# Optimization experiments

Measured on AMD Instinct MI355X. Metric: run time of the kernel, lower is better.

## Reference

```python
import jax, jax.numpy as jnp
import numpy as np

D_MODEL = 512
HEADS = 8
FF_HIDDEN = 1024
EPS = 1e-6


def setup_inputs() -> dict:
    key = jax.random.key(0)
    ks = jax.random.split(key, 12)
    s = 1.0 / np.sqrt(D_MODEL)
    inp = {
        'x': jax.random.normal(ks[0], (2, 4096, D_MODEL), dtype=jnp.float32),
        'Wq': jax.random.normal(ks[1], (D_MODEL, D_MODEL), dtype=jnp.float32) * s,
        'bq': jnp.zeros((D_MODEL,), jnp.float32),
        'Wk': jax.random.normal(ks[2], (D_MODEL, D_MODEL), dtype=jnp.float32) * s,
        'bk': jnp.zeros((D_MODEL,), jnp.float32),
        'Wv': jax.random.normal(ks[3], (D_MODEL, D_MODEL), dtype=jnp.float32) * s,
        'bv': jnp.zeros((D_MODEL,), jnp.float32),
        'Wo': jax.random.normal(ks[4], (D_MODEL, D_MODEL), dtype=jnp.float32) * s,
        'bo': jnp.zeros((D_MODEL,), jnp.float32),
        'a1': jnp.ones((D_MODEL,), jnp.float32),
        'b1': jnp.zeros((D_MODEL,), jnp.float32),
        'a2': jnp.ones((D_MODEL,), jnp.float32),
        'b2': jnp.zeros((D_MODEL,), jnp.float32),
        'W1': jax.random.normal(ks[5], (D_MODEL, FF_HIDDEN), dtype=jnp.float32) * s,
        'c1': jnp.zeros((FF_HIDDEN,), jnp.float32),
        'W2': jax.random.normal(ks[6], (FF_HIDDEN, D_MODEL), dtype=jnp.float32) * (1.0 / np.sqrt(FF_HIDDEN)),
        'c2': jnp.zeros((D_MODEL,), jnp.float32),
    }
    return inp


def _layer_norm(x, a, b):
    # Faithful to source: uses unbiased std (torch default) and divides by (std + eps)
    mean = jnp.mean(x, axis=-1, keepdims=True)
    std = jnp.std(x, axis=-1, keepdims=True, ddof=1)
    return a * ((x - mean) / (std + EPS)) + b


def _encoder_block(x, Wq, bq, Wk, bk, Wv, bv, Wo, bo, a1, b1, a2, b2, W1, c1, W2, c2):
    B, S, D = x.shape
    H, dk = HEADS, D // HEADS
    q = (x @ Wq + bq).reshape(B, S, H, dk).transpose(0, 2, 1, 3)  # [B,H,S,dk]
    k = (x @ Wk + bk).reshape(B, S, H, dk).transpose(0, 2, 1, 3)
    v = (x @ Wv + bv).reshape(B, S, H, dk).transpose(0, 2, 1, 3)
    scores = jnp.einsum('bhqd,bhkd->bhqk', q, k) / np.sqrt(dk)
    probs = jax.nn.softmax(scores, axis=-1)
    attn = jnp.einsum('bhqk,bhkd->bhqd', probs, v)
    concat = attn.transpose(0, 2, 1, 3).reshape(B, S, D)
    attn_out = concat @ Wo + bo
    x = _layer_norm(x + attn_out, a1, b1)  # dropout = identity (eval mode)
    ffn = jax.nn.relu(x @ W1 + c1) @ W2 + c2
    return _layer_norm(x + ffn, a2, b2)


def reference(x, Wq, bq, Wk, bk, Wv, bv, Wo, bo, a1, b1, a2, b2, W1, c1, W2, c2):
    return _encoder_block(x, Wq, bq, Wk, bk, Wv, bv, Wo, bo, a1, b1, a2, b2, W1, c1, W2, c2)
```

## Files before the change

kernel.cpp:

```cpp
#include <hip/hip_runtime.h>
#include <stdint.h>

typedef short short8 __attribute__((ext_vector_type(8)));
typedef short short4v __attribute__((ext_vector_type(4)));
typedef float f32x4 __attribute__((ext_vector_type(4)));
typedef float f32x16 __attribute__((ext_vector_type(16)));
typedef unsigned int u32x4 __attribute__((ext_vector_type(4)));

#define LOG2E 1.44269504088896f
#define QSCALE (0.125f * LOG2E)

__device__ __forceinline__ unsigned short f2b(float f) {
  union { float f; unsigned int u; } x; x.f = f;
  unsigned int u = x.u;
  unsigned int r = (u + 0x7fffu + ((u >> 16) & 1u)) >> 16;
  return (unsigned short)r;
}
__device__ __forceinline__ float b2f(unsigned short s) {
  union { unsigned int u; float f; } x; x.u = ((unsigned int)s) << 16;
  return x.f;
}
__device__ __forceinline__ void gl16(const void* g, void* l) {
  __builtin_amdgcn_global_load_lds((const __attribute__((address_space(1))) void*)g,
                                   (__attribute__((address_space(3))) void*)l, 16, 0, 0);
}
__device__ __forceinline__ unsigned int cvtpk(float lo, float hi) {
  unsigned int r;
  asm("v_cvt_pk_bf16_f32 %0, %1, %2" : "=v"(r) : "v"(lo), "v"(hi));
  return r;
}
__device__ __forceinline__ void plswap(unsigned int& a, unsigned int& b) {
  asm volatile("v_permlane32_swap_b32 %0, %1" : "+v"(a), "+v"(b));
}

__global__ __launch_bounds__(256) void castx_k(const float* __restrict__ X,
                                               unsigned short* __restrict__ Xb) {
  int i = blockIdx.x * 256 + threadIdx.x;
  const float* p = X + (size_t)i * 8;
  float4 a = *(const float4*)(p);
  float4 b = *(const float4*)(p + 4);
  short8 o;
  o[0] = (short)f2b(a.x); o[1] = (short)f2b(a.y);
  o[2] = (short)f2b(a.z); o[3] = (short)f2b(a.w);
  o[4] = (short)f2b(b.x); o[5] = (short)f2b(b.y);
  o[6] = (short)f2b(b.z); o[7] = (short)f2b(b.w);
  *(short8*)(Xb + (size_t)i * 8) = o;
}

__global__ __launch_bounds__(256) void catb_k(const float* __restrict__ bq,
                                              const float* __restrict__ bk,
                                              const float* __restrict__ bv,
                                              float* __restrict__ Bqkv) {
  for (int i = threadIdx.x; i < 1536; i += 256) {
    float v = (i < 512) ? bq[i] * QSCALE : (i < 1024 ? bk[i - 512] : bv[i - 1024]);
    Bqkv[i] = v;
  }
}

__global__ __launch_bounds__(256) void wtrans_k(const float* __restrict__ W,
                                                unsigned short* __restrict__ WT,
                                                int K, int N, float scale) {
  __shared__ float t[64][65];
  int k0 = blockIdx.x * 64, n0 = blockIdx.y * 64;
  for (int i = threadIdx.x; i < 4096; i += 256) {
    int r = i >> 6, c = i & 63;
    t[r][c] = W[(size_t)(k0 + r) * N + n0 + c];
  }
  __syncthreads();
  for (int i = threadIdx.x; i < 4096; i += 256) {
    int r = i >> 6, c = i & 63;
    WT[(size_t)(n0 + r) * K + k0 + c] = f2b(t[c][r] * scale);
  }
}

template <int EPI>
__global__ __launch_bounds__(256) void gemm_bt(
    const unsigned short* __restrict__ A, const unsigned short* __restrict__ BT,
    const float* __restrict__ bias, float* __restrict__ Cf,
    unsigned short* __restrict__ Cb, int M, int N, int K) {
  __shared__ unsigned short As[128 * 32];
  __shared__ unsigned short Bs[128 * 32];
  int t = threadIdx.x, w = t >> 6, l = t & 63;
  int bm = blockIdx.x, bn = blockIdx.y;
  int wm = w >> 1, wn = w & 1;
  int g = l >> 4, ln = l & 15;
  f32x4 acc[4][4] = {};
  const unsigned short* Arow = A + (size_t)bm * 128 * K;
  const unsigned short* Brow = BT + (size_t)bn * 128 * K;
  int nk = K >> 5;
  for (int kt = 0; kt < nk; ++kt) {
    int k0 = kt * 32;
#pragma unroll
    for (int i = 0; i < 2; ++i) {
      int cl = i * 256 + t;
      int r = cl >> 2, c = cl & 3;
      char* ldsA = (char*)As + (size_t)(i * 256 + w * 64) * 16;
      char* ldsB = (char*)Bs + (size_t)(i * 256 + w * 64) * 16;
      gl16(Arow + (size_t)r * K + k0 + c * 8, ldsA);
      gl16(Brow + (size_t)r * K + k0 + c * 8, ldsB);
    }
    __syncthreads();
    short8 af[4], bf[4];
    int ko = g * 8;
#pragma unroll
    for (int i = 0; i < 4; ++i)
      af[i] = *(const short8*)&As[(wm * 64 + i * 16 + ln) * 32 + ko];
#pragma unroll
    for (int j = 0; j < 4; ++j)
      bf[j] = *(const short8*)&Bs[(wn * 64 + j * 16 + ln) * 32 + ko];
    __builtin_amdgcn_s_setprio(1);
#pragma unroll
    for (int i = 0; i < 4; ++i)
#pragma unroll
      for (int j = 0; j < 4; ++j)
        acc[i][j] = __builtin_amdgcn_mfma_f32_16x16x32_bf16(af[i], bf[j], acc[i][j], 0, 0, 0);
    __builtin_amdgcn_s_setprio(0);
    __syncthreads();
  }
#pragma unroll
  for (int i = 0; i < 4; ++i) {
    int row = bm * 128 + wm * 64 + i * 16 + g * 4;
#pragma unroll
    for (int j = 0; j < 4; ++j) {
      int col = bn * 128 + wn * 64 + j * 16 + ln;
      float bv = bias[col];
      float vv[4];
#pragma unroll
      for (int r = 0; r < 4; ++r) {
        float v = acc[i][j][r] + bv;
        if constexpr (EPI == 2) v = v > 0.f ? v : 0.f;
        vv[r] = v;
      }
      if constexpr (EPI == 3) {
        if (col < 1024) {
#pragma unroll
          for (int r = 0; r < 4; ++r)
            Cb[(size_t)(col >> 9) * 4194304 + (size_t)(row + r) * 512 + (col & 511)] = f2b(vv[r]);
        } else {
          short4v pk;
#pragma unroll
          for (int r = 0; r < 4; ++r) pk[r] = (short)f2b(vv[r]);
          *(short4v*)((unsigned short*)Cf +
                      (size_t)((row >> 12) * 512 + (col & 511)) * 4096 + (row & 4095)) = pk;
        }
      } else {
#pragma unroll
        for (int r = 0; r < 4; ++r)
          Cb[(size_t)(row + r) * N + col] = f2b(vv[r]);
      }
    }
  }
}

template <bool WB>
__global__ __launch_bounds__(512) void gemmln_k(
    const unsigned short* __restrict__ A, const unsigned short* __restrict__ BT,
    const float* __restrict__ bias, const float* __restrict__ X,
    const float* __restrict__ gamma, const float* __restrict__ beta,
    float* __restrict__ outf, unsigned short* __restrict__ outb, int K) {
  __shared__ unsigned short As[16 * 32];
  __shared__ unsigned short Bs[512 * 32];
  __shared__ float stats[8][16][2];
  __shared__ float minv[16][2];
  int tid = threadIdx.x, wv = tid >> 6, lane = tid & 63;
  int g = lane >> 4, ln = lane & 15;
  int bm = blockIdx.x;
  f32x4 acc[4] = {};
  const unsigned short* Arow = A + (size_t)bm * 16 * K;
  int nk = K >> 5;
  for (int kt = 0; kt < nk; ++kt) {
    int k0 = kt * 32;
    if (tid < 64) {
      int r = tid >> 2, c = tid & 3;
      gl16(Arow + (size_t)r * K + k0 + c * 8, (char*)As + tid * 16);
    }
#pragma unroll
    for (int i = 0; i < 4; ++i) {
      int u = i * 512 + tid;
      int r = u >> 2, c = u & 3;
      gl16(BT + (size_t)r * K + k0 + c * 8, (char*)Bs + (size_t)u * 16);
    }
    __syncthreads();
    short8 af = *(const short8*)&As[ln * 32 + g * 8];
    __builtin_amdgcn_s_setprio(1);
#pragma unroll
    for (int j = 0; j < 4; ++j) {
      short8 bf = *(const short8*)&Bs[(wv * 64 + j * 16 + ln) * 32 + g * 8];
      acc[j] = __builtin_amdgcn_mfma_f32_16x16x32_bf16(af, bf, acc[j], 0, 0, 0);
    }
    __builtin_amdgcn_s_setprio(0);
    __syncthreads();
  }
  int row0 = bm * 16;
  float v[4][4];
  float ps[4] = {0.f, 0.f, 0.f, 0.f}, pss[4] = {0.f, 0.f, 0.f, 0.f};
#pragma unroll
  for (int j = 0; j < 4; ++j) {
    int col = wv * 64 + j * 16 + ln;
    float bv = bias[col];
#pragma unroll
    for (int r = 0; r < 4; ++r) {
      float t = acc[j][r] + bv + X[(size_t)(row0 + g * 4 + r) * 512 + col];
      v[j][r] = t;
      ps[r] += t; pss[r] += t * t;
    }
  }
#pragma unroll
  for (int off = 1; off < 16; off <<= 1) {
#pragma unroll
    for (int r = 0; r < 4; ++r) {
      ps[r] += __shfl_xor(ps[r], off);
      pss[r] += __shfl_xor(pss[r], off);
    }
  }
  if (ln == 0) {
#pragma unroll
    for (int r = 0; r < 4; ++r) {
      stats[wv][g * 4 + r][0] = ps[r];
      stats[wv][g * 4 + r][1] = pss[r];
    }
  }
  __syncthreads();
  if (tid < 16) {
    float S = 0.f, SS = 0.f;
#pragma unroll
    for (int w2 = 0; w2 < 8; ++w2) { S += stats[w2][tid][0]; SS += stats[w2][tid][1]; }
    float mean = S * (1.f / 512.f);
    float var = fmaxf((SS - 512.f * mean * mean) * (1.f / 511.f), 0.f);
    minv[tid][0] = mean;
    minv[tid][1] = 1.f / (sqrtf(var) + 1e-6f);
  }
  __syncthreads();
#pragma unroll
  for (int j = 0; j < 4; ++j) {
    int col = wv * 64 + j * 16 + ln;
    float gm = gamma[col], bt2 = beta[col];
#pragma unroll
    for (int r = 0; r < 4; ++r) {
      int row = g * 4 + r;
      float o = gm * ((v[j][r] - minv[row][0]) * minv[row][1]) + bt2;
      outf[(size_t)(row0 + row) * 512 + col] = o;
      if constexpr (WB) outb[(size_t)(row0 + row) * 512 + col] = f2b(o);
    }
  }
}

__global__ __launch_bounds__(256, 2) void attn_k(
    const unsigned short* __restrict__ Q, const unsigned short* __restrict__ Kb,
    const unsigned short* __restrict__ Vt, unsigned short* __restrict__ Opart,
    float* __restrict__ L) {
  __shared__ unsigned short Ks[2][4096];
  __shared__ unsigned short Vs[3][4096];
  int tid = threadIdx.x, wv = tid >> 6, lane = tid & 63;
  int l31 = lane & 31, hi = lane >> 5;
  int qb = blockIdx.x, bh = blockIdx.y, z = blockIdx.z;
  int b = bh >> 3, h = bh & 7;
  int q0 = qb * 256 + wv * 64;
  int kvbase = z * 2048;

  short8 qfA[4], qfB[4];
  {
    const unsigned short* qpA = Q + (size_t)(b * 4096 + q0 + l31) * 512 + h * 64;
    const unsigned short* qpB = qpA + 32 * 512;
#pragma unroll
    for (int ks = 0; ks < 4; ++ks) {
      qfA[ks] = *(const short8*)(qpA + ks * 16 + hi * 8);
      qfB[ks] = *(const short8*)(qpB + ks * 16 + hi * 8);
    }
  }

  short8 ones;
#pragma unroll
  for (int j = 0; j < 8; ++j) ones[j] = (short)0x3F80;

  const f32x16 Z = {};
  f32x16 oA0 = {}, oA1 = {}, oB0 = {}, oB1 = {}, laccA = {}, laccB = {};

  int skk[2], sc[2];
#pragma unroll
  for (int i = 0; i < 2; ++i) {
    int u = i * 256 + tid;
    int r2 = u >> 4, s = u & 15;
    skk[i] = 2 * r2 + (s & 1);
    sc[i] = ((s >> 1) ^ (r2 & 7)) * 8;
  }

  auto stage = [&](char* kb_lds, char* vb_lds, int kv) {
    const unsigned short* ksrc = Kb + (size_t)(b * 4096 + kv) * 512 + h * 64;
    const unsigned short* vsrc = Vt + (size_t)(bh * 64) * 4096 + kv;
#pragma unroll
    for (int i = 0; i < 2; ++i) {
      gl16(ksrc + (size_t)skk[i] * 512 + sc[i], kb_lds + (size_t)(i * 256 + wv * 64) * 16);
      gl16(vsrc + (size_t)skk[i] * 4096 + sc[i], vb_lds + (size_t)(i * 256 + wv * 64) * 16);
    }
  };

  int r2a = l31 >> 1, par = l31 & 1, perm = r2a & 7;
  int rdb = r2a * 256 + (par << 4);

  auto qk = [&](const char* kbase, f32x16& sA0, f32x16& sA1, f32x16& sB0, f32x16& sB1) {
    __builtin_amdgcn_s_setprio(1);
#pragma unroll
    for (int ks = 0; ks < 4; ++ks) {
      int c16 = ks * 2 + hi;
      int byteA = rdb + (((c16 ^ perm) << 1) << 4);
      short8 k0 = *(const short8*)(kbase + byteA);
      short8 k1 = *(const short8*)(kbase + byteA + 4096);
      if (ks == 0) {
        sA0 = __builtin_amdgcn_mfma_f32_32x32x16_bf16(k0, qfA[0], Z, 0, 0, 0);
        sA1 = __builtin_amdgcn_mfma_f32_32x32x16_bf16(k1, qfA[0], Z, 0, 0, 0);
        sB0 = __builtin_amdgcn_mfma_f32_32x32x16_bf16(k0, qfB[0], Z, 0, 0, 0);
        sB1 = __builtin_amdgcn_mfma_f32_32x32x16_bf16(k1, qfB[0], Z, 0, 0, 0);
      } else {
        sA0 = __builtin_amdgcn_mfma_f32_32x32x16_bf16(k0, qfA[ks], sA0, 0, 0, 0);
        sA1 = __builtin_amdgcn_mfma_f32_32x32x16_bf16(k1, qfA[ks], sA1, 0, 0, 0);
        sB0 = __builtin_amdgcn_mfma_f32_32x32x16_bf16(k0, qfB[ks], sB0, 0, 0, 0);
        sB1 = __builtin_amdgcn_mfma_f32_32x32x16_bf16(k1, qfB[ks], sB1, 0, 0, 0);
      }
    }
    __builtin_amdgcn_s_setprio(0);
  };

  auto pv = [&](const char* vbase, const short8* pfA, const short8* pfB) {
    __builtin_amdgcn_s_setprio(1);
#pragma unroll
    for (int ks = 0; ks < 4; ++ks) {
      int c16 = ks * 2 + hi;
      int byteA = rdb + (((c16 ^ perm) << 1) << 4);
      short8 v0 = *(const short8*)(vbase + byteA);
      short8 v1 = *(const short8*)(vbase + byteA + 4096);
      oA0 = __builtin_amdgcn_mfma_f32_32x32x16_bf16(v0, pfA[ks], oA0, 0, 0, 0);
      oA1 = __builtin_amdgcn_mfma_f32_32x32x16_bf16(v1, pfA[ks], oA1, 0, 0, 0);
      oB0 = __builtin_amdgcn_mfma_f32_32x32x16_bf16(v0, pfB[ks], oB0, 0, 0, 0);
      oB1 = __builtin_amdgcn_mfma_f32_32x32x16_bf16(v1, pfB[ks], oB1, 0, 0, 0);
      laccA = __builtin_amdgcn_mfma_f32_32x32x16_bf16(ones, pfA[ks], laccA, 0, 0, 0);
      laccB = __builtin_amdgcn_mfma_f32_32x32x16_bf16(ones, pfB[ks], laccB, 0, 0, 0);
    }
    __builtin_amdgcn_s_setprio(0);
  };

  auto exppack = [&](f32x16& s0, f32x16& s1, short8* pf) {
#pragma unroll
    for (int r = 0; r < 16; ++r) s0[r] = __builtin_amdgcn_exp2f(s0[r]);
#pragma unroll
    for (int r = 0; r < 16; ++r) s1[r] = __builtin_amdgcn_exp2f(s1[r]);
    unsigned int u0 = cvtpk(s0[0], s0[1]), u1 = cvtpk(s0[4], s0[5]);
    plswap(u0, u1);
    unsigned int u2 = cvtpk(s0[2], s0[3]), u3 = cvtpk(s0[6], s0[7]);
    plswap(u2, u3);
    unsigned int u4 = cvtpk(s0[8], s0[9]), u5 = cvtpk(s0[12], s0[13]);
    plswap(u4, u5);
    unsigned int u6 = cvtpk(s0[10], s0[11]), u7 = cvtpk(s0[14], s0[15]);
    plswap(u6, u7);
    union { u32x4 u; short8 s; } cv;
    cv.u = (u32x4){u0, u2, u1, u3}; pf[0] = cv.s;
    cv.u = (u32x4){u4, u6, u5, u7}; pf[1] = cv.s;
    unsigned int w0 = cvtpk(s1[0], s1[1]), w1 = cvtpk(s1[4], s1[5]);
    plswap(w0, w1);
    unsigned int w2 = cvtpk(s1[2], s1[3]), w3 = cvtpk(s1[6], s1[7]);
    plswap(w2, w3);
    unsigned int w4 = cvtpk(s1[8], s1[9]), w5 = cvtpk(s1[12], s1[13]);
    plswap(w4, w5);
    unsigned int w6 = cvtpk(s1[10], s1[11]), w7 = cvtpk(s1[14], s1[15]);
    plswap(w6, w7);
    cv.u = (u32x4){w0, w2, w1, w3}; pf[2] = cv.s;
    cv.u = (u32x4){w4, w6, w5, w7}; pf[3] = cv.s;
  };

  char* k0b = (char*)&Ks[0][0];
  char* k1b = (char*)&Ks[1][0];
  char* vA = (char*)&Vs[0][0];
  char* vB = (char*)&Vs[1][0];
  char* vC = (char*)&Vs[2][0];
  stage(k0b, vA, kvbase);
  __syncthreads();
  stage(k1b, vB, kvbase + 64);

  f32x16 sA0, sA1, sB0, sB1;
  qk(k0b, sA0, sA1, sB0, sB1);
  short8 pfA[4], pfB[4];
  exppack(sA0, sA1, pfA);
  exppack(sB0, sB1, pfB);

#pragma unroll 1
  for (int t = 1; t < 32; ++t) {
    __syncthreads();
    char* kr = (t & 1) ? k1b : k0b;
    char* kw = (t & 1) ? k0b : k1b;
    if (t < 31) stage(kw, vC, kvbase + (t + 1) * 64);
    qk(kr, sA0, sA1, sB0, sB1);
    pv(vA, pfA, pfB);
    exppack(sA0, sA1, pfA);
    exppack(sB0, sB1, pfB);
    char* tmp = vA; vA = vB; vB = vC; vC = tmp;
  }
  pv(vA, pfA, pfB);

  int plane = z * 16 + bh;
  unsigned short* op = Opart + (size_t)plane * 262144;
  int qA = q0 + l31, qB = q0 + 32 + l31;
#pragma unroll
  for (int r = 0; r < 16; ++r) {
    int dr = (r & 3) + 8 * (r >> 2) + 4 * hi;
    op[(size_t)dr * 4096 + qA] = f2b(oA0[r]);
    op[(size_t)(dr + 32) * 4096 + qA] = f2b(oA1[r]);
    op[(size_t)dr * 4096 + qB] = f2b(oB0[r]);
    op[(size_t)(dr + 32) * 4096 + qB] = f2b(oB1[r]);
  }
  if (hi == 0) {
    L[(size_t)plane * 4096 + qA] = laccA[0];
    L[(size_t)plane * 4096 + qB] = laccB[0];
  }
}

__global__ __launch_bounds__(256) void comb_k(const unsigned short* __restrict__ Opart,
                                              const float* __restrict__ L,
                                              unsigned short* __restrict__ O) {
  __shared__ float sli[64];
  __shared__ unsigned short tt[64][80];
  int tid = threadIdx.x;
  int qt = blockIdx.x, bh = blockIdx.y;
  int b = bh >> 3, h = bh & 7;
  int q0 = qt * 64;
  if (tid < 64) {
    int q = q0 + tid;
    sli[tid] = 1.0f / (L[(size_t)bh * 4096 + q] + L[(size_t)(16 + bh) * 4096 + q]);
  }
  __syncthreads();
  const unsigned short* p0 = Opart + (size_t)bh * 262144;
  const unsigned short* p1 = Opart + (size_t)(16 + bh) * 262144;
  int d = tid >> 2, qg = tid & 3;
#pragma unroll
  for (int i = 0; i < 16; ++i) {
    int qq = qg * 16 + i;
    size_t idx = (size_t)d * 4096 + q0 + qq;
    tt[qq][d] = f2b((b2f(p0[idx]) + b2f(p1[idx])) * sli[qq]);
  }
  __syncthreads();
  int qr = tid >> 2, dc = tid & 3;
  short8 v0 = *(const short8*)&tt[qr][dc * 16];
  short8 v1 = *(const short8*)&tt[qr][dc * 16 + 8];
  size_t row = (size_t)(b * 4096 + q0 + qr);
  *(short8*)(O + row * 512 + h * 64 + dc * 16) = v0;
  *(short8*)(O + row * 512 + h * 64 + dc * 16 + 8) = v1;
}

extern "C" void kernel_launch(void* const* d_in, const int* in_sizes, int n_in,
                              void* d_out, int out_size, void* d_ws, size_t ws_size,
                              hipStream_t stream) {
  const float* x  = (const float*)d_in[0];
  const float* Wq = (const float*)d_in[1];
  const float* bq = (const float*)d_in[2];
  const float* Wk = (const float*)d_in[3];
  const float* bk = (const float*)d_in[4];
  const float* Wv = (const float*)d_in[5];
  const float* bv = (const float*)d_in[6];
  const float* Wo = (const float*)d_in[7];
  const float* bo = (const float*)d_in[8];
  const float* a1 = (const float*)d_in[9];
  const float* b1 = (const float*)d_in[10];
  const float* a2 = (const float*)d_in[11];
  const float* b2 = (const float*)d_in[12];
  const float* W1 = (const float*)d_in[13];
  const float* c1 = (const float*)d_in[14];
  const float* W2 = (const float*)d_in[15];
  const float* c2 = (const float*)d_in[16];

  char* ws = (char*)d_ws;
  const size_t MB = 1024 * 1024;
  unsigned short* Xb  = (unsigned short*)(ws + 0);
  unsigned short* Qb  = (unsigned short*)(ws + 8 * MB);
  unsigned short* Kbf = (unsigned short*)(ws + 16 * MB);
  float* L = (float*)(ws + 24 * MB);
  unsigned short* Vtb = (unsigned short*)(ws + 32 * MB);
  unsigned short* WqkvT = (unsigned short*)(ws + 40 * MB);
  unsigned short* WoT = (unsigned short*)(ws + 41 * MB + 512 * 1024);
  unsigned short* W1T = (unsigned short*)(ws + 42 * MB);
  unsigned short* W2T = (unsigned short*)(ws + 43 * MB);
  unsigned short* Opart = (unsigned short*)(ws + 44 * MB);
  float* Bqkv = (float*)(ws + 44 * MB);
  float* Y1 = (float*)(ws + 60 * MB);
  unsigned short* Att = Xb;
  unsigned short* Y1b = Qb;
  unsigned short* Hb  = Kbf;

  castx_k<<<2048, 256, 0, stream>>>(x, Xb);
  catb_k<<<1, 256, 0, stream>>>(bq, bk, bv, Bqkv);
  wtrans_k<<<dim3(8, 8), 256, 0, stream>>>(Wq, WqkvT, 512, 512, QSCALE);
  wtrans_k<<<dim3(8, 8), 256, 0, stream>>>(Wk, WqkvT + 512 * 512, 512, 512, 1.0f);
  wtrans_k<<<dim3(8, 8), 256, 0, stream>>>(Wv, WqkvT + 2 * 512 * 512, 512, 512, 1.0f);
  wtrans_k<<<dim3(8, 8), 256, 0, stream>>>(Wo, WoT, 512, 512, 1.0f);
  wtrans_k<<<dim3(8, 16), 256, 0, stream>>>(W1, W1T, 512, 1024, 1.0f);
  wtrans_k<<<dim3(16, 8), 256, 0, stream>>>(W2, W2T, 1024, 512, 1.0f);

  gemm_bt<3><<<dim3(64, 12), 256, 0, stream>>>(Xb, WqkvT, Bqkv, (float*)Vtb, Qb, 8192, 1536, 512);

  attn_k<<<dim3(16, 16, 2), 256, 0, stream>>>(Qb, Kbf, Vtb, Opart, L);
  comb_k<<<dim3(64, 16), 256, 0, stream>>>(Opart, L, Att);

  gemmln_k<true><<<512, 512, 0, stream>>>(Att, WoT, bo, x, a1, b1, Y1, Y1b, 512);
  gemm_bt<2><<<dim3(64, 8), 256, 0, stream>>>(Y1b, W1T, c1, nullptr, Hb, 8192, 1024, 512);
  gemmln_k<false><<<512, 512, 0, stream>>>(Hb, W2T, c2, Y1, a2, b2, (float*)d_out, nullptr, 1024);
}
```

Baseline: 222.6 us.

## Fuse prep kernels into one launch and double row tile in GEMM+LayerNorm

The cast, bias-concat and six weight-transpose kernels are merged into one prep kernel that dispatches on block index, so eight launches become one. The fused GEMM+LayerNorm kernel now handles 32 rows per block instead of 16, reusing each loaded weight tile for twice as many MFMAs and halving weight traffic per row. The cost is fewer blocks (256 instead of 512) and more registers per thread, which may lower parallelism and occupancy on this GPU.

```diff
diff --git a/kernel.cpp b/kernel.cpp
--- a/kernel.cpp
+++ b/kernel.cpp
@@ -33,41 +33,60 @@
   asm volatile("v_permlane32_swap_b32 %0, %1" : "+v"(a), "+v"(b));
 }
 
-__global__ __launch_bounds__(256) void castx_k(const float* __restrict__ X,
-                                               unsigned short* __restrict__ Xb) {
-  int i = blockIdx.x * 256 + threadIdx.x;
-  const float* p = X + (size_t)i * 8;
-  float4 a = *(const float4*)(p);
-  float4 b = *(const float4*)(p + 4);
-  short8 o;
-  o[0] = (short)f2b(a.x); o[1] = (short)f2b(a.y);
-  o[2] = (short)f2b(a.z); o[3] = (short)f2b(a.w);
-  o[4] = (short)f2b(b.x); o[5] = (short)f2b(b.y);
-  o[6] = (short)f2b(b.z); o[7] = (short)f2b(b.w);
-  *(short8*)(Xb + (size_t)i * 8) = o;
-}
-
-__global__ __launch_bounds__(256) void catb_k(const float* __restrict__ bq,
-                                              const float* __restrict__ bk,
-                                              const float* __restrict__ bv,
-                                              float* __restrict__ Bqkv) {
-  for (int i = threadIdx.x; i < 1536; i += 256) {
-    float v = (i < 512) ? bq[i] * QSCALE : (i < 1024 ? bk[i - 512] : bv[i - 1024]);
-    Bqkv[i] = v;
-  }
-}
-
-__global__ __launch_bounds__(256) void wtrans_k(const float* __restrict__ W,
-                                                unsigned short* __restrict__ WT,
-                                                int K, int N, float scale) {
+__global__ __launch_bounds__(256) void prep_k(
+    const float* __restrict__ X, unsigned short* __restrict__ Xb,
+    const float* __restrict__ Wq, const float* __restrict__ Wk,
+    const float* __restrict__ Wv, const float* __restrict__ Wo,
+    const float* __restrict__ W1, const float* __restrict__ W2,
+    unsigned short* __restrict__ WqkvT, unsigned short* __restrict__ WoT,
+    unsigned short* __restrict__ W1T, unsigned short* __restrict__ W2T,
+    const float* __restrict__ bq, const float* __restrict__ bk,
+    const float* __restrict__ bv, float* __restrict__ Bqkv) {
   __shared__ float t[64][65];
-  int k0 = blockIdx.x * 64, n0 = blockIdx.y * 64;
-  for (int i = threadIdx.x; i < 4096; i += 256) {
+  int bid = blockIdx.x, tid = threadIdx.x;
+  if (bid < 2048) {
+    int i = bid * 256 + tid;
+    const float* p = X + (size_t)i * 8;
+    float4 a = *(const float4*)(p);
+    float4 b = *(const float4*)(p + 4);
+    short8 o;
+    o[0] = (short)f2b(a.x); o[1] = (short)f2b(a.y);
+    o[2] = (short)f2b(a.z); o[3] = (short)f2b(a.w);
+    o[4] = (short)f2b(b.x); o[5] = (short)f2b(b.y);
+    o[6] = (short)f2b(b.z); o[7] = (short)f2b(b.w);
+    *(short8*)(Xb + (size_t)i * 8) = o;
+    return;
+  }
+  if (bid == 2560) {
+    for (int i = tid; i < 1536; i += 256) {
+      float v = (i < 512) ? bq[i] * QSCALE : (i < 1024 ? bk[i - 512] : bv[i - 1024]);
+      Bqkv[i] = v;
+    }
+    return;
+  }
+  int idx = bid - 2048;
+  const float* W; unsigned short* WT; int K, N, kb, nb; float scale = 1.0f;
+  if (idx < 256) {
+    int sec = idx >> 6, local = idx & 63;
+    K = 512; N = 512; kb = local >> 3; nb = local & 7;
+    if (sec == 0) { W = Wq; WT = WqkvT; scale = QSCALE; }
+    else if (sec == 1) { W = Wk; WT = WqkvT + 512 * 512; }
+    else if (sec == 2) { W = Wv; WT = WqkvT + 2 * 512 * 512; }
+    else { W = Wo; WT = WoT; }
+  } else if (idx < 384) {
+    int local = idx - 256; K = 512; N = 1024; kb = local >> 4; nb = local & 15;
+    W = W1; WT = W1T;
+  } else {
+    int local = idx - 384; K = 1024; N = 512; kb = local >> 3; nb = local & 7;
+    W = W2; WT = W2T;
+  }
+  int k0 = kb * 64, n0 = nb * 64;
+  for (int i = tid; i < 4096; i += 256) {
     int r = i >> 6, c = i & 63;
     t[r][c] = W[(size_t)(k0 + r) * N + n0 + c];
   }
   __syncthreads();
-  for (int i = threadIdx.x; i < 4096; i += 256) {
+  for (int i = tid; i < 4096; i += 256) {
     int r = i >> 6, c = i & 63;
     WT[(size_t)(n0 + r) * K + k0 + c] = f2b(t[c][r] * scale);
   }
@@ -158,19 +177,19 @@
     const float* __restrict__ bias, const float* __restrict__ X,
     const float* __restrict__ gamma, const float* __restrict__ beta,
     float* __restrict__ outf, unsigned short* __restrict__ outb, int K) {
-  __shared__ unsigned short As[16 * 32];
+  __shared__ unsigned short As[32 * 32];
   __shared__ unsigned short Bs[512 * 32];
-  __shared__ float stats[8][16][2];
-  __shared__ float minv[16][2];
+  __shared__ float stats[8][32][2];
+  __shared__ float minv[32][2];
   int tid = threadIdx.x, wv = tid >> 6, lane = tid & 63;
   int g = lane >> 4, ln = lane & 15;
   int bm = blockIdx.x;
-  f32x4 acc[4] = {};
-  const unsigned short* Arow = A + (size_t)bm * 16 * K;
+  f32x4 acc[2][4] = {};
+  const unsigned short* Arow = A + (size_t)bm * 32 * K;
   int nk = K >> 5;
   for (int kt = 0; kt < nk; ++kt) {
     int k0 = kt * 32;
-    if (tid < 64) {
+    if (tid < 128) {
       int r = tid >> 2, c = tid & 3;
       gl16(Arow + (size_t)r * K + k0 + c * 8, (char*)As + tid * 16);
     }
@@ -181,47 +200,60 @@
       gl16(BT + (size_t)r * K + k0 + c * 8, (char*)Bs + (size_t)u * 16);
     }
     __syncthreads();
-    short8 af = *(const short8*)&As[ln * 32 + g * 8];
+    short8 af[2], bf[4];
+#pragma unroll
+    for (int i = 0; i < 2; ++i)
+      af[i] = *(const short8*)&As[(i * 16 + ln) * 32 + g * 8];
+#pragma unroll
+    for (int j = 0; j < 4; ++j)
+      bf[j] = *(const short8*)&Bs[(wv * 64 + j * 16 + ln) * 32 + g * 8];
     __builtin_amdgcn_s_setprio(1);
 #pragma unroll
-    for (int j = 0; j < 4; ++j) {
-      short8 bf = *(const short8*)&Bs[(wv * 64 + j * 16 + ln) * 32 + g * 8];
-      acc[j] = __builtin_amdgcn_mfma_f32_16x16x32_bf16(af, bf, acc[j], 0, 0, 0);
-    }
+    for (int i = 0; i < 2; ++i)
+#pragma unroll
+      for (int j = 0; j < 4; ++j)
+        acc[i][j] = __builtin_amdgcn_mfma_f32_16x16x32_bf16(af[i], bf[j], acc[i][j], 0, 0, 0);
     __builtin_amdgcn_s_setprio(0);
     __syncthreads();
   }
-  int row0 = bm * 16;
-  float v[4][4];
-  float ps[4] = {0.f, 0.f, 0.f, 0.f}, pss[4] = {0.f, 0.f, 0.f, 0.f};
-#pragma unroll
-  for (int j = 0; j < 4; ++j) {
-    int col = wv * 64 + j * 16 + ln;
-    float bv = bias[col];
-#pragma unroll
-    for (int r = 0; r < 4; ++r) {
-      float t = acc[j][r] + bv + X[(size_t)(row0 + g * 4 + r) * 512 + col];
-      v[j][r] = t;
-      ps[r] += t; pss[r] += t * t;
-    }
-  }
+  int row0 = bm * 32;
+  float v[2][4][4];
+  float ps[8], pss[8];
+#pragma unroll
+  for (int k = 0; k < 8; ++k) { ps[k] = 0.f; pss[k] = 0.f; }
+#pragma unroll
+  for (int i = 0; i < 2; ++i)
+#pragma unroll
+    for (int j = 0; j < 4; ++j) {
+      int col = wv * 64 + j * 16 + ln;
+      float bv = bias[col];
+#pragma unroll
+      for (int r = 0; r < 4; ++r) {
+        int row = i * 16 + g * 4 + r;
+        float t = acc[i][j][r] + bv + X[(size_t)(row0 + row) * 512 + col];
+        v[i][j][r] = t;
+        ps[i * 4 + r] += t; pss[i * 4 + r] += t * t;
+      }
+    }
 #pragma unroll
   for (int off = 1; off < 16; off <<= 1) {
 #pragma unroll
-    for (int r = 0; r < 4; ++r) {
-      ps[r] += __shfl_xor(ps[r], off);
-      pss[r] += __shfl_xor(pss[r], off);
+    for (int k = 0; k < 8; ++k) {
+      ps[k] += __shfl_xor(ps[k], off);
+      pss[k] += __shfl_xor(pss[k], off);
     }
   }
   if (ln == 0) {
 #pragma unroll
-    for (int r = 0; r < 4; ++r) {
-      stats[wv][g * 4 + r][0] = ps[r];
-      stats[wv][g * 4 + r][1] = pss[r];
-    }
+    for (int i = 0; i < 2; ++i)
+#pragma unroll
+      for (int r = 0; r < 4; ++r) {
+        stats[wv][i * 16 + g * 4 + r][0] = ps[i * 4 + r];
+        stats[wv][i * 16 + g * 4 + r][1] = pss[i * 4 + r];
+      }
   }
   __syncthreads();
-  if (tid < 16) {
+  if (tid < 32) {
     float S = 0.f, SS = 0.f;
 #pragma unroll
     for (int w2 = 0; w2 < 8; ++w2) { S += stats[w2][tid][0]; SS += stats[w2][tid][1]; }
@@ -232,17 +264,19 @@
   }
   __syncthreads();
 #pragma unroll
-  for (int j = 0; j < 4; ++j) {
-    int col = wv * 64 + j * 16 + ln;
-    float gm = gamma[col], bt2 = beta[col];
-#pragma unroll
-    for (int r = 0; r < 4; ++r) {
-      int row = g * 4 + r;
-      float o = gm * ((v[j][r] - minv[row][0]) * minv[row][1]) + bt2;
-      outf[(size_t)(row0 + row) * 512 + col] = o;
-      if constexpr (WB) outb[(size_t)(row0 + row) * 512 + col] = f2b(o);
-    }
-  }
+  for (int i = 0; i < 2; ++i)
+#pragma unroll
+    for (int j = 0; j < 4; ++j) {
+      int col = wv * 64 + j * 16 + ln;
+      float gm = gamma[col], bt2 = beta[col];
+#pragma unroll
+      for (int r = 0; r < 4; ++r) {
+        int row = i * 16 + g * 4 + r;
+        float o = gm * ((v[i][j][r] - minv[row][0]) * minv[row][1]) + bt2;
+        outf[(size_t)(row0 + row) * 512 + col] = o;
+        if constexpr (WB) outb[(size_t)(row0 + row) * 512 + col] = f2b(o);
+      }
+    }
 }
 
 __global__ __launch_bounds__(256, 2) void attn_k(
@@ -484,21 +518,15 @@
   unsigned short* Y1b = Qb;
   unsigned short* Hb  = Kbf;
 
-  castx_k<<<2048, 256, 0, stream>>>(x, Xb);
-  catb_k<<<1, 256, 0, stream>>>(bq, bk, bv, Bqkv);
-  wtrans_k<<<dim3(8, 8), 256, 0, stream>>>(Wq, WqkvT, 512, 512, QSCALE);
-  wtrans_k<<<dim3(8, 8), 256, 0, stream>>>(Wk, WqkvT + 512 * 512, 512, 512, 1.0f);
-  wtrans_k<<<dim3(8, 8), 256, 0, stream>>>(Wv, WqkvT + 2 * 512 * 512, 512, 512, 1.0f);
-  wtrans_k<<<dim3(8, 8), 256, 0, stream>>>(Wo, WoT, 512, 512, 1.0f);
-  wtrans_k<<<dim3(8, 16), 256, 0, stream>>>(W1, W1T, 512, 1024, 1.0f);
-  wtrans_k<<<dim3(16, 8), 256, 0, stream>>>(W2, W2T, 1024, 512, 1.0f);
+  prep_k<<<2561, 256, 0, stream>>>(x, Xb, Wq, Wk, Wv, Wo, W1, W2,
+                                   WqkvT, WoT, W1T, W2T, bq, bk, bv, Bqkv);
 
   gemm_bt<3><<<dim3(64, 12), 256, 0, stream>>>(Xb, WqkvT, Bqkv, (float*)Vtb, Qb, 8192, 1536, 512);
 
   attn_k<<<dim3(16, 16, 2), 256, 0, stream>>>(Qb, Kbf, Vtb, Opart, L);
   comb_k<<<dim3(64, 16), 256, 0, stream>>>(Opart, L, Att);
 
-  gemmln_k<true><<<512, 512, 0, stream>>>(Att, WoT, bo, x, a1, b1, Y1, Y1b, 512);
+  gemmln_k<true><<<256, 512, 0, stream>>>(Att, WoT, bo, x, a1, b1, Y1, Y1b, 512);
   gemm_bt<2><<<dim3(64, 8), 256, 0, stream>>>(Y1b, W1T, c1, nullptr, Hb, 8192, 1024, 512);
-  gemmln_k<false><<<512, 512, 0, stream>>>(Hb, W2T, c2, Y1, a2, b2, (float*)d_out, nullptr, 1024);
-}
+  gemmln_k<false><<<256, 512, 0, stream>>>(Hb, W2T, c2, Y1, a2, b2, (float*)d_out, nullptr, 1024);
+}
```

After: 194.8 us. -12.5%, faster.
